# Kernel tuning notes

Hardware: AMD Instinct MI355X
Metric: run time of the kernel (lower is better)

## Reference

```python
import jax, jax.numpy as jnp
import numpy as np

NEG_SLOPE = 0.2  # PyG GATConv default leaky_relu negative_slope


def gat_conv(x, edge_index, W, att_src, att_dst, bias, heads, out_ch):
    """PyG GATConv (add_self_loops=False, concat=True, dropout disabled)."""
    N = x.shape[0]
    src, dst = edge_index[0], edge_index[1]
    h = (x @ W).reshape(N, heads, out_ch)               # [N,H,C]
    a_src = jnp.einsum('nhc,hc->nh', h, att_src)        # [N,H]
    a_dst = jnp.einsum('nhc,hc->nh', h, att_dst)        # [N,H]
    e = jax.nn.leaky_relu(a_src[src] + a_dst[dst], NEG_SLOPE)  # [E,H]
    # segment softmax over edges grouped by destination node
    e_max = jax.ops.segment_max(e, dst, num_segments=N)  # [N,H]
    e_exp = jnp.exp(e - e_max[dst])
    denom = jax.ops.segment_sum(e_exp, dst, num_segments=N)
    alpha = e_exp / (denom[dst] + 1e-16)                 # [E,H]
    msg = h[src] * alpha[:, :, None]                     # [E,H,C]
    out = jax.ops.segment_sum(msg, dst, num_segments=N)  # [N,H,C]
    return out.reshape(N, heads * out_ch) + bias


def setup_inputs() -> dict:
    key = jax.random.key(0)
    ks = jax.random.split(key, 10)
    N, E, F_IN, H, C1, OUT = 50000, 1600000, 256, 8, 8, 64
    s = 0.1
    return {
        'x': jax.random.normal(ks[0], (N, F_IN), jnp.float32),
        'edge_index': jax.random.randint(ks[1], (2, E), 0, N, jnp.int64),
        'W1': jax.random.normal(ks[2], (F_IN, H * C1), jnp.float32) * s,
        'att_src1': jax.random.normal(ks[3], (H, C1), jnp.float32) * s,
        'att_dst1': jax.random.normal(ks[4], (H, C1), jnp.float32) * s,
        'bias1': jax.random.normal(ks[5], (H * C1,), jnp.float32) * s,
        'W2': jax.random.normal(ks[6], (H * C1, OUT), jnp.float32) * s,
        'att_src2': jax.random.normal(ks[7], (1, OUT), jnp.float32) * s,
        'att_dst2': jax.random.normal(ks[8], (1, OUT), jnp.float32) * s,
        'bias2': jax.random.normal(ks[9], (OUT,), jnp.float32) * s,
    }


def reference(x, edge_index, W1, att_src1, att_dst1, bias1, W2, att_src2, att_dst2, bias2):
    # GAT.forward, eval mode with disable_dropout=True (no dropout, no loss)
    h = gat_conv(x, edge_index, W1, att_src1, att_dst1, bias1, heads=8, out_ch=8)
    h = jax.nn.elu(h)
    h = gat_conv(h, edge_index, W2, att_src2, att_dst2, bias2, heads=1, out_ch=64)
    return jax.nn.log_softmax(h, axis=1)
```

## Files before the change

kernel.cpp:

```cpp
#include <hip/hip_runtime.h>
#include <math.h>

#define LRELU 0.2f
#define BSH 7
#define BSZ (1 << BSH)
#define CH 8192
#define ECH 2048
#define GB 10
#define CAP 5120

typedef __attribute__((ext_vector_type(8))) short bf16x8;
typedef __attribute__((ext_vector_type(4))) float f32x4;

static __device__ __forceinline__ float bf2f(unsigned int u16) {
    union { unsigned int i; float f; } c; c.i = u16 << 16; return c.f;
}
static __device__ __forceinline__ unsigned short f2bf(float f) {
    union { float f; unsigned int i; } c; c.f = f;
    unsigned int x = c.i;
    return (unsigned short)((x + 0x7fffu + ((x >> 16) & 1u)) >> 16);
}


__global__ __launch_bounds__(256) void k_prep(const float* __restrict__ W1,
                                              const float* __restrict__ W2,
                                              const float* __restrict__ as2in,
                                              const float* __restrict__ ad2in,
                                              unsigned short* __restrict__ Wt1,
                                              unsigned short* __restrict__ Wt2,
                                              unsigned short* __restrict__ h1b,
                                              unsigned short* __restrict__ gb,
                                              float* __restrict__ w2s,
                                              float* __restrict__ w2d,
                                              int* __restrict__ bcur,
                                              int N, int NB) {
    int idx = blockIdx.x * 256 + threadIdx.x;
    if (idx < 16384) {
        int n = idx >> 8, k = idx & 255;
        Wt1[idx] = f2bf(W1[k * 64 + n]);
    } else if (idx < 16384 + 4096) {
        int j = idx - 16384;
        int n = j >> 6, k = j & 63;
        Wt2[j] = f2bf(W2[k * 64 + n]);
    } else if (idx >= 20480 && idx < 20544) {
        h1b[(size_t)N * 64 + (idx - 20480)] = 0;
    } else if (idx >= 20544 && idx < 20608) {
        gb[(size_t)N * 64 + (idx - 20544)] = 0;
    } else if (idx >= 20608 && idx < 20672) {
        int c = idx - 20608;
        float s = 0.f;
#pragma unroll
        for (int n = 0; n < 64; ++n) s += W2[c * 64 + n] * as2in[n];
        w2s[c] = s;
    } else if (idx >= 20672 && idx < 20736) {
        int c = idx - 20672;
        float s = 0.f;
#pragma unroll
        for (int n = 0; n < 64; ++n) s += W2[c * 64 + n] * ad2in[n];
        w2d[c] = s;
    } else if (idx >= 20736 && idx < 20736 + NB) {
        int b = idx - 20736;
        bcur[b] = b * CAP;
    }
}


__global__ __launch_bounds__(256) void k_mid(const int* __restrict__ src,
                                             const int* __restrict__ dstArr,
                                             int E, int NB,
                                             int* __restrict__ bcur,
                                             unsigned* __restrict__ pairs,
                                             const float* __restrict__ X,
                                             const unsigned short* __restrict__ Wt,
                                             const float* __restrict__ attd,
                                             int N, unsigned short* __restrict__ Hb,
                                             float* __restrict__ adst,
                                             int nchunk) {
    __shared__ short Xl[64 * 256];
    __shared__ int cnt2[512];
    int t = threadIdx.x;
    if ((int)blockIdx.x < nchunk) {
        int* lds_d = (int*)Xl;
        int e0 = blockIdx.x * CH;
        int e1 = e0 + CH; if (e1 > E) e1 = E;
        int n = e1 - e0;
        for (int b = t; b < 512; b += 256) cnt2[b] = 0;
        __syncthreads();
        for (int i = t; i < n; i += 256) {
            int d = dstArr[e0 + i];
            lds_d[i] = d;
            atomicAdd(&cnt2[d >> BSH], 1);
        }
        __syncthreads();
        for (int b = t; b < NB; b += 256) {
            int c = cnt2[b];
            cnt2[b] = c ? atomicAdd(&bcur[b], c) : 0;
        }
        __syncthreads();
        for (int i = t; i < n; i += 256) {
            int d = lds_d[i];
            int p = atomicAdd(&cnt2[d >> BSH], 1);
            pairs[p] = ((unsigned)src[e0 + i] << BSH) | (unsigned)(d & (BSZ - 1));
        }
        return;
    }
    int bx = (int)blockIdx.x - nchunk;
    int l = t & 63, w = t >> 6;
    int rblk = bx * 64;

    int half = l >> 5;
    int c8 = (l & 31) * 8;
#pragma unroll
    for (int i = 0; i < 8; ++i) {
        int rl = w * 16 + i * 2 + half;
        int row = rblk + rl;
        float4 x0 = {0.f, 0.f, 0.f, 0.f}, x1 = {0.f, 0.f, 0.f, 0.f};
        if (row < N) {
            x0 = *reinterpret_cast<const float4*>(X + (size_t)row * 256 + c8);
            x1 = *reinterpret_cast<const float4*>(X + (size_t)row * 256 + c8 + 4);
        }
        bf16x8 p;
        p[0] = (short)f2bf(x0.x); p[1] = (short)f2bf(x0.y);
        p[2] = (short)f2bf(x0.z); p[3] = (short)f2bf(x0.w);
        p[4] = (short)f2bf(x1.x); p[5] = (short)f2bf(x1.y);
        p[6] = (short)f2bf(x1.z); p[7] = (short)f2bf(x1.w);
        int g = (l & 31) ^ (rl & 7);
        *reinterpret_cast<bf16x8*>(&Xl[rl * 256 + g * 8]) = p;
    }
    __syncthreads();

    int m = l & 15, quad = l >> 4;
    int rl = w * 16 + m;
    f32x4 acc0 = {0.f, 0.f, 0.f, 0.f}, acc1 = acc0, acc2 = acc0, acc3 = acc0;
#pragma unroll
    for (int tt = 0; tt < 8; ++tt) {
        int g = (tt * 4 + quad) ^ (m & 7);
        bf16x8 a = *reinterpret_cast<const bf16x8*>(&Xl[rl * 256 + g * 8]);
        int kk = tt * 32 + quad * 8;
        bf16x8 b0 = *reinterpret_cast<const bf16x8*>(&Wt[(0 * 16 + m) * 256 + kk]);
        bf16x8 b1 = *reinterpret_cast<const bf16x8*>(&Wt[(1 * 16 + m) * 256 + kk]);
        bf16x8 b2 = *reinterpret_cast<const bf16x8*>(&Wt[(2 * 16 + m) * 256 + kk]);
        bf16x8 b3 = *reinterpret_cast<const bf16x8*>(&Wt[(3 * 16 + m) * 256 + kk]);
        acc0 = __builtin_amdgcn_mfma_f32_16x16x32_bf16(a, b0, acc0, 0, 0, 0);
        acc1 = __builtin_amdgcn_mfma_f32_16x16x32_bf16(a, b1, acc1, 0, 0, 0);
        acc2 = __builtin_amdgcn_mfma_f32_16x16x32_bf16(a, b2, acc2, 0, 0, 0);
        acc3 = __builtin_amdgcn_mfma_f32_16x16x32_bf16(a, b3, acc3, 0, 0, 0);
    }

    int r0 = rblk + w * 16;
    f32x4 accs[4] = {acc0, acc1, acc2, acc3};
#pragma unroll
    for (int nt = 0; nt < 4; ++nt) {
        int cn = nt * 16 + m;
        float av_d = attd[cn];
#pragma unroll
        for (int r = 0; r < 4; ++r) {
            int row = r0 + quad * 4 + r;
            float hv = accs[nt][r];
            if (row < N) Hb[(size_t)row * 64 + cn] = f2bf(hv);
            float vd = hv * av_d;
            vd += __shfl_xor(vd, 1, 64); vd += __shfl_xor(vd, 2, 64); vd += __shfl_xor(vd, 4, 64);
            if ((m & 7) == 0 && row < N) {
                adst[row * 8 + (cn >> 3)] = vd;
            }
        }
    }
}


__global__ __launch_bounds__(256) void k_bucket(const int* __restrict__ bcur,
                                                const unsigned* __restrict__ pairs,
                                                int N, int* __restrict__ rowptr,
                                                int* __restrict__ rowend,
                                                int* __restrict__ col) {
    __shared__ int pairsS[CAP];
    __shared__ int cnt[BSZ];
    __shared__ int cur[BSZ];
    int t = threadIdx.x;
    int b = blockIdx.x;
    int dlo = b << BSH;
    int dhi = dlo + BSZ; if (dhi > N) dhi = N;
    int nd = dhi - dlo;
    int jb = b * CAP;
    int je = bcur[b];
    int n = je - jb;
    if (t < BSZ) cnt[t] = 0;
    __syncthreads();
    for (int i = t; i < n; i += 256) {
        int pk = (int)pairs[jb + i];
        pairsS[i] = pk;
        atomicAdd(&cnt[pk & (BSZ - 1)], 1);
    }
    __syncthreads();
    if (t < 64) {
        int v0 = cnt[t], v1 = cnt[64 + t];
        int i0 = v0;
#pragma unroll
        for (int off = 1; off < 64; off <<= 1) {
            int q = __shfl_up(i0, off, 64);
            if (t >= off) i0 += q;
        }
        int tot0 = __shfl(i0, 63, 64);
        int i1 = v1;
#pragma unroll
        for (int off = 1; off < 64; off <<= 1) {
            int q = __shfl_up(i1, off, 64);
            if (t >= off) i1 += q;
        }
        int e0x = jb + i0 - v0;
        int e1x = jb + tot0 + i1 - v1;
        cur[t] = e0x;
        cur[64 + t] = e1x;
        if (t < nd) { rowptr[dlo + t] = e0x; rowend[dlo + t] = jb + i0; }
        if (64 + t < nd) { rowptr[dlo + 64 + t] = e1x; rowend[dlo + 64 + t] = jb + tot0 + i1; }
    }
    __syncthreads();
    for (int i = t; i < n; i += 256) {
        int pk = pairsS[i];
        int p = atomicAdd(&cur[pk & (BSZ - 1)], 1);
        col[p] = pk >> BSH;
    }
}


__global__ __launch_bounds__(256) void k_gather1f(const int* __restrict__ rowptr,
                                                  const int* __restrict__ rowend,
                                                  const int* __restrict__ col,
                                                  const uint4* __restrict__ Hb8,
                                                  const float* __restrict__ adst,
                                                  const float* __restrict__ attS,
                                                  const float* __restrict__ bias,
                                                  const unsigned short* __restrict__ Wt2,
                                                  const float* __restrict__ w2d,
                                                  int N,
                                                  unsigned short* __restrict__ Gb,
                                                  float* __restrict__ ad2) {
    __shared__ int colS[ECH];
    __shared__ short h2l[32 * 64];
    int t = threadIdx.x;
    int gid = t >> 3, sub = t & 7;
    int d0 = blockIdx.x * 32;
    int dend = d0 + 32; if (dend > N) dend = N;
    int d = d0 + gid;
    int dok = (d < dend);
    int dc = dok ? d : d0;
    int jb = rowptr[dc];
    int je = rowend[dc];
    if (!dok) { jb = 0; je = 0; }
    float adv = dok ? adst[dc * 8 + sub] : 0.f;
    float aS[8];
#pragma unroll
    for (int c = 0; c < 8; ++c) aS[c] = attS[sub * 8 + c];
    int ebeg = rowptr[d0];
    int eend = rowend[dend - 1];

    float acc[8] = {0.f, 0.f, 0.f, 0.f, 0.f, 0.f, 0.f, 0.f};
    float denom = 0.f;
    for (int cb = ebeg; cb < eend; cb += ECH) {
        int ce = cb + ECH; if (ce > eend) ce = eend;
        int n = ce - cb;
        __syncthreads();
        for (int i = t; i < n; i += 256) colS[i] = col[cb + i];
        __syncthreads();
        int lo = (jb > cb) ? jb : cb;
        int hi = (je < ce) ? je : ce;
        for (int u = lo; u < hi; u += GB) {
            uint4 hv8[GB];
#pragma unroll
            for (int q = 0; q < GB; ++q) {
                int uu = u + q;
                int s = (uu < hi) ? colS[uu - cb] : N;
                hv8[q] = Hb8[(size_t)s * 8 + sub];
            }
            __builtin_amdgcn_sched_barrier(0);
#pragma unroll
            for (int q = 0; q < GB; ++q) {
                uint4 hv = hv8[q];
                float f0 = bf2f(hv.x & 0xffffu), f1 = bf2f(hv.x >> 16);
                float f2 = bf2f(hv.y & 0xffffu), f3 = bf2f(hv.y >> 16);
                float f4 = bf2f(hv.z & 0xffffu), f5 = bf2f(hv.z >> 16);
                float f6 = bf2f(hv.w & 0xffffu), f7 = bf2f(hv.w >> 16);
                float ps = f0 * aS[0];
                ps = fmaf(f1, aS[1], ps); ps = fmaf(f2, aS[2], ps);
                ps = fmaf(f3, aS[3], ps); ps = fmaf(f4, aS[4], ps);
                ps = fmaf(f5, aS[5], ps); ps = fmaf(f6, aS[6], ps);
                ps = fmaf(f7, aS[7], ps);
                float e = ps + adv;
                e = (e > 0.f) ? e : LRELU * e;
                float wgt = ((u + q) < hi) ? __expf(e) : 0.f;
                denom += wgt;
                acc[0] = fmaf(wgt, f0, acc[0]); acc[1] = fmaf(wgt, f1, acc[1]);
                acc[2] = fmaf(wgt, f2, acc[2]); acc[3] = fmaf(wgt, f3, acc[3]);
                acc[4] = fmaf(wgt, f4, acc[4]); acc[5] = fmaf(wgt, f5, acc[5]);
                acc[6] = fmaf(wgt, f6, acc[6]); acc[7] = fmaf(wgt, f7, acc[7]);
            }
        }
    }

    float invd = 1.f / (denom + 1e-16f);
    float v[8];
#pragma unroll
    for (int c = 0; c < 8; ++c) {
        float x = fmaf(acc[c], invd, bias[sub * 8 + c]);
        v[c] = (x > 0.f) ? x : expm1f(x);
    }
    float vd = 0.f;
#pragma unroll
    for (int c = 0; c < 8; ++c) vd = fmaf(v[c], w2d[sub * 8 + c], vd);
    vd += __shfl_xor(vd, 1, 64); vd += __shfl_xor(vd, 2, 64); vd += __shfl_xor(vd, 4, 64);
    if (dok && sub == 0) ad2[d] = vd;

    bf16x8 p;
#pragma unroll
    for (int c = 0; c < 8; ++c) p[c] = (short)f2bf(v[c]);
    *reinterpret_cast<bf16x8*>(&h2l[gid * 64 + (sub ^ (gid & 7)) * 8]) = p;
    __syncthreads();

    int l = t & 63, w = t >> 6;
    int m = l & 15, quad = l >> 4;
    int mt = w & 1;
    int ntb = (w >> 1) * 2;
    int r = mt * 16 + m;
    f32x4 g0 = {0.f, 0.f, 0.f, 0.f}, g1 = g0;
#pragma unroll
    for (int tt = 0; tt < 2; ++tt) {
        bf16x8 a = *reinterpret_cast<const bf16x8*>(
            &h2l[r * 64 + ((tt * 4 + quad) ^ (r & 7)) * 8]);
        int kk = tt * 32 + quad * 8;
        bf16x8 b0 = *reinterpret_cast<const bf16x8*>(&Wt2[((ntb + 0) * 16 + m) * 64 + kk]);
        bf16x8 b1 = *reinterpret_cast<const bf16x8*>(&Wt2[((ntb + 1) * 16 + m) * 64 + kk]);
        g0 = __builtin_amdgcn_mfma_f32_16x16x32_bf16(a, b0, g0, 0, 0, 0);
        g1 = __builtin_amdgcn_mfma_f32_16x16x32_bf16(a, b1, g1, 0, 0, 0);
    }
    f32x4 gs[2] = {g0, g1};
#pragma unroll
    for (int nt = 0; nt < 2; ++nt) {
        int cn = (ntb + nt) * 16 + m;
#pragma unroll
        for (int rr = 0; rr < 4; ++rr) {
            int dr = d0 + mt * 16 + quad * 4 + rr;
            if (dr < N) Gb[(size_t)dr * 64 + cn] = f2bf(gs[nt][rr]);
        }
    }
}


__global__ __launch_bounds__(256) void k_gather2(const int* __restrict__ rowptr,
                                                 const int* __restrict__ rowend,
                                                 const int* __restrict__ col,
                                                 const uint4* __restrict__ Gb8,
                                                 const float* __restrict__ adst,
                                                 const float* __restrict__ w2s,
                                                 const float* __restrict__ bias,
                                                 int N,
                                                 float* __restrict__ out) {
    __shared__ int colS[ECH];
    int t = threadIdx.x;
    int gid = t >> 3, sub = t & 7;
    int d0 = blockIdx.x * 32;
    int dend = d0 + 32; if (dend > N) dend = N;
    int d = d0 + gid;
    int dok = (d < dend);
    int dc = dok ? d : d0;
    int jb = rowptr[dc];
    int je = rowend[dc];
    if (!dok) { jb = 0; je = 0; }
    float adv = dok ? adst[dc] : 0.f;
    float wS[8];
#pragma unroll
    for (int c = 0; c < 8; ++c) wS[c] = w2s[sub * 8 + c];
    int ebeg = rowptr[d0];
    int eend = rowend[dend - 1];

    float acc[8] = {0.f, 0.f, 0.f, 0.f, 0.f, 0.f, 0.f, 0.f};
    float denom = 0.f;
    for (int cb = ebeg; cb < eend; cb += ECH) {
        int ce = cb + ECH; if (ce > eend) ce = eend;
        int n = ce - cb;
        __syncthreads();
        for (int i = t; i < n; i += 256) colS[i] = col[cb + i];
        __syncthreads();
        int lo = (jb > cb) ? jb : cb;
        int hi = (je < ce) ? je : ce;
        for (int u = lo; u < hi; u += GB) {
            uint4 hv8[GB];
#pragma unroll
            for (int q = 0; q < GB; ++q) {
                int uu = u + q;
                int s = (uu < hi) ? colS[uu - cb] : N;
                hv8[q] = Gb8[(size_t)s * 8 + sub];
            }
            __builtin_amdgcn_sched_barrier(0);
#pragma unroll
            for (int q = 0; q < GB; ++q) {
                uint4 hv = hv8[q];
                float f0 = bf2f(hv.x & 0xffffu), f1 = bf2f(hv.x >> 16);
                float f2 = bf2f(hv.y & 0xffffu), f3 = bf2f(hv.y >> 16);
                float f4 = bf2f(hv.z & 0xffffu), f5 = bf2f(hv.z >> 16);
                float f6 = bf2f(hv.w & 0xffffu), f7 = bf2f(hv.w >> 16);
                float ps = f0 * wS[0];
                ps = fmaf(f1, wS[1], ps); ps = fmaf(f2, wS[2], ps);
                ps = fmaf(f3, wS[3], ps); ps = fmaf(f4, wS[4], ps);
                ps = fmaf(f5, wS[5], ps); ps = fmaf(f6, wS[6], ps);
                ps = fmaf(f7, wS[7], ps);
                ps += __shfl_xor(ps, 1, 64);
                ps += __shfl_xor(ps, 2, 64);
                ps += __shfl_xor(ps, 4, 64);
                float e = ps + adv;
                e = (e > 0.f) ? e : LRELU * e;
                float wgt = ((u + q) < hi) ? __expf(e) : 0.f;
                denom += wgt;
                acc[0] = fmaf(wgt, f0, acc[0]); acc[1] = fmaf(wgt, f1, acc[1]);
                acc[2] = fmaf(wgt, f2, acc[2]); acc[3] = fmaf(wgt, f3, acc[3]);
                acc[4] = fmaf(wgt, f4, acc[4]); acc[5] = fmaf(wgt, f5, acc[5]);
                acc[6] = fmaf(wgt, f6, acc[6]); acc[7] = fmaf(wgt, f7, acc[7]);
            }
        }
    }
    float invd = 1.f / (denom + 1e-16f);
    float v[8];
#pragma unroll
    for (int c = 0; c < 8; ++c) v[c] = fmaf(acc[c], invd, bias[sub * 8 + c]);
    float m = v[0];
#pragma unroll
    for (int c = 1; c < 8; ++c) m = fmaxf(m, v[c]);
    m = fmaxf(m, __shfl_xor(m, 1, 64));
    m = fmaxf(m, __shfl_xor(m, 2, 64));
    m = fmaxf(m, __shfl_xor(m, 4, 64));
    float se = 0.f;
#pragma unroll
    for (int c = 0; c < 8; ++c) se += __expf(v[c] - m);
    se += __shfl_xor(se, 1, 64);
    se += __shfl_xor(se, 2, 64);
    se += __shfl_xor(se, 4, 64);
    float ls = m + __logf(se);
    if (dok) {
        float4 o0, o1;
        o0.x = v[0] - ls; o0.y = v[1] - ls; o0.z = v[2] - ls; o0.w = v[3] - ls;
        o1.x = v[4] - ls; o1.y = v[5] - ls; o1.z = v[6] - ls; o1.w = v[7] - ls;
        *reinterpret_cast<float4*>(&out[(size_t)d * 64 + sub * 8]) = o0;
        *reinterpret_cast<float4*>(&out[(size_t)d * 64 + sub * 8 + 4]) = o1;
    }
}


extern "C" void kernel_launch(void* const* d_in, const int* in_sizes, int n_in,
                              void* d_out, int out_size, void* d_ws, size_t ws_size,
                              hipStream_t stream) {
    const float* x   = (const float*)d_in[0];
    const int*   ei  = (const int*)d_in[1];
    const float* W1  = (const float*)d_in[2];
    const float* as1 = (const float*)d_in[3];
    const float* ad1 = (const float*)d_in[4];
    const float* b1  = (const float*)d_in[5];
    const float* W2  = (const float*)d_in[6];
    const float* as2 = (const float*)d_in[7];
    const float* ad2 = (const float*)d_in[8];
    const float* b2  = (const float*)d_in[9];
    float* out = (float*)d_out;

    const int N = in_sizes[0] / 256;
    const int E = in_sizes[1] / 2;
    const int* src = ei;
    const int* dst = ei + E;
    const int NB = (N + BSZ - 1) >> BSH;
    const int nchunk = (E + CH - 1) / CH;

    char* ws = (char*)d_ws;
    size_t off = 0;
    auto alloc = [&](size_t bytes) -> void* {
        void* p = ws + off;
        off = (off + bytes + 255) & ~(size_t)255;
        return p;
    };
    int*      bcur   = (int*)alloc((size_t)NB * 4);
    int*      rowptr = (int*)alloc((size_t)N * 4);
    int*      rowend = (int*)alloc((size_t)N * 4);
    int*      col    = (int*)alloc((size_t)NB * CAP * 4);
    unsigned* pairs  = (unsigned*)alloc((size_t)NB * CAP * 4);
    unsigned short* wt1 = (unsigned short*)alloc(64 * 256 * 2);
    unsigned short* wt2 = (unsigned short*)alloc(64 * 64 * 2);
    unsigned short* h1b = (unsigned short*)alloc((size_t)(N + 1) * 64 * 2);
    float* a_d1   = (float*)alloc((size_t)N * 8 * 4);
    unsigned short* gb  = (unsigned short*)alloc((size_t)(N + 1) * 64 * 2);
    float* a_d2   = (float*)alloc((size_t)N * 4);
    float* w2s    = (float*)alloc(64 * 4);
    float* w2d    = (float*)alloc(64 * 4);
    (void)ws_size; (void)n_in; (void)out_size;

    int prep_blocks = (20736 + NB + 255) / 256;
    k_prep<<<prep_blocks, 256, 0, stream>>>(W1, W2, as2, ad2, wt1, wt2,
                                            h1b, gb, w2s, w2d, bcur, N, NB);

    int gblk = (N + 63) / 64;
    k_mid<<<nchunk + gblk, 256, 0, stream>>>(src, dst, E, NB, bcur, pairs,
                                             x, wt1, ad1, N, h1b, a_d1, nchunk);

    k_bucket<<<NB, 256, 0, stream>>>(bcur, pairs, N, rowptr, rowend, col);

    int gather_blocks = (N + 31) / 32;
    k_gather1f<<<gather_blocks, 256, 0, stream>>>(rowptr, rowend, col,
                                                  (const uint4*)h1b,
                                                  a_d1, as1, b1, wt2, w2d,
                                                  N, gb, a_d2);

    k_gather2<<<gather_blocks, 256, 0, stream>>>(rowptr, rowend, col,
                                                 (const uint4*)gb,
                                                 a_d2, w2s, b2, N, out);
}
```

Measured before the change: 225.9 us.

## Fuse per-bucket CSR sort into both gather kernels and drop k_bucket

Removes the separate bucketing kernel that built rowptr, rowend and col arrays in global memory. Each gather block now owns a 32-node destination bucket: it loads that bucket's packed (src, dst) pairs, counts and prefix-sums them in LDS, and scatters the source indices into an LDS column list before gathering. This saves a kernel launch and the global write and re-read of the CSR arrays. In exchange the in-LDS sort is done twice (once per layer), k_mid issues more global bucket-counter atomics because there are more, smaller buckets, and the fixed per-bucket capacity of 1408 assumes no bucket overflows.

```diff
diff --git a/kernel.cpp b/kernel.cpp
--- a/kernel.cpp
+++ b/kernel.cpp
@@ -2,12 +2,12 @@
 #include <math.h>
 
 #define LRELU 0.2f
-#define BSH 7
+#define BSH 5
 #define BSZ (1 << BSH)
 #define CH 8192
-#define ECH 2048
 #define GB 10
-#define CAP 5120
+#define CAP 1408
+#define NBMAX 1600
 
 typedef __attribute__((ext_vector_type(8))) short bf16x8;
 typedef __attribute__((ext_vector_type(4))) float f32x4;
@@ -77,14 +77,14 @@
                                              float* __restrict__ adst,
                                              int nchunk) {
     __shared__ short Xl[64 * 256];
-    __shared__ int cnt2[512];
+    __shared__ int cnt2[NBMAX];
     int t = threadIdx.x;
     if ((int)blockIdx.x < nchunk) {
         int* lds_d = (int*)Xl;
         int e0 = blockIdx.x * CH;
         int e1 = e0 + CH; if (e1 > E) e1 = E;
         int n = e1 - e0;
-        for (int b = t; b < 512; b += 256) cnt2[b] = 0;
+        for (int b = t; b < NBMAX; b += 256) cnt2[b] = 0;
         __syncthreads();
         for (int i = t; i < n; i += 256) {
             int d = dstArr[e0 + i];
@@ -168,64 +168,8 @@
 }
 
 
-__global__ __launch_bounds__(256) void k_bucket(const int* __restrict__ bcur,
-                                                const unsigned* __restrict__ pairs,
-                                                int N, int* __restrict__ rowptr,
-                                                int* __restrict__ rowend,
-                                                int* __restrict__ col) {
-    __shared__ int pairsS[CAP];
-    __shared__ int cnt[BSZ];
-    __shared__ int cur[BSZ];
-    int t = threadIdx.x;
-    int b = blockIdx.x;
-    int dlo = b << BSH;
-    int dhi = dlo + BSZ; if (dhi > N) dhi = N;
-    int nd = dhi - dlo;
-    int jb = b * CAP;
-    int je = bcur[b];
-    int n = je - jb;
-    if (t < BSZ) cnt[t] = 0;
-    __syncthreads();
-    for (int i = t; i < n; i += 256) {
-        int pk = (int)pairs[jb + i];
-        pairsS[i] = pk;
-        atomicAdd(&cnt[pk & (BSZ - 1)], 1);
-    }
-    __syncthreads();
-    if (t < 64) {
-        int v0 = cnt[t], v1 = cnt[64 + t];
-        int i0 = v0;
-#pragma unroll
-        for (int off = 1; off < 64; off <<= 1) {
-            int q = __shfl_up(i0, off, 64);
-            if (t >= off) i0 += q;
-        }
-        int tot0 = __shfl(i0, 63, 64);
-        int i1 = v1;
-#pragma unroll
-        for (int off = 1; off < 64; off <<= 1) {
-            int q = __shfl_up(i1, off, 64);
-            if (t >= off) i1 += q;
-        }
-        int e0x = jb + i0 - v0;
-        int e1x = jb + tot0 + i1 - v1;
-        cur[t] = e0x;
-        cur[64 + t] = e1x;
-        if (t < nd) { rowptr[dlo + t] = e0x; rowend[dlo + t] = jb + i0; }
-        if (64 + t < nd) { rowptr[dlo + 64 + t] = e1x; rowend[dlo + 64 + t] = jb + tot0 + i1; }
-    }
-    __syncthreads();
-    for (int i = t; i < n; i += 256) {
-        int pk = pairsS[i];
-        int p = atomicAdd(&cur[pk & (BSZ - 1)], 1);
-        col[p] = pk >> BSH;
-    }
-}
-
-
-__global__ __launch_bounds__(256) void k_gather1f(const int* __restrict__ rowptr,
-                                                  const int* __restrict__ rowend,
-                                                  const int* __restrict__ col,
+__global__ __launch_bounds__(256) void k_gather1f(const int* __restrict__ bcur,
+                                                  const unsigned* __restrict__ pairs,
                                                   const uint4* __restrict__ Hb8,
                                                   const float* __restrict__ adst,
                                                   const float* __restrict__ attS,
@@ -235,65 +179,86 @@
                                                   int N,
                                                   unsigned short* __restrict__ Gb,
                                                   float* __restrict__ ad2) {
-    __shared__ int colS[ECH];
+    __shared__ int pairsS[CAP];
+    __shared__ int colT[CAP];
+    __shared__ int cntS[BSZ];
+    __shared__ int baseS[BSZ];
+    __shared__ int curS[BSZ];
     __shared__ short h2l[32 * 64];
     int t = threadIdx.x;
     int gid = t >> 3, sub = t & 7;
-    int d0 = blockIdx.x * 32;
-    int dend = d0 + 32; if (dend > N) dend = N;
+    int b = blockIdx.x;
+    int d0 = b << BSH;
     int d = d0 + gid;
-    int dok = (d < dend);
+    int dok = (d < N);
     int dc = dok ? d : d0;
-    int jb = rowptr[dc];
-    int je = rowend[dc];
-    if (!dok) { jb = 0; je = 0; }
     float adv = dok ? adst[dc * 8 + sub] : 0.f;
     float aS[8];
 #pragma unroll
     for (int c = 0; c < 8; ++c) aS[c] = attS[sub * 8 + c];
-    int ebeg = rowptr[d0];
-    int eend = rowend[dend - 1];
+
+    int jb = b * CAP;
+    int n = bcur[b] - jb;
+    if (t < BSZ) cntS[t] = 0;
+    __syncthreads();
+    for (int i = t; i < n; i += 256) {
+        int pk = (int)pairs[jb + i];
+        pairsS[i] = pk;
+        atomicAdd(&cntS[pk & (BSZ - 1)], 1);
+    }
+    __syncthreads();
+    if (t < 64) {
+        int v = (t < BSZ) ? cntS[t] : 0;
+        int inc = v;
+#pragma unroll
+        for (int off = 1; off < BSZ; off <<= 1) {
+            int q = __shfl_up(inc, off, 64);
+            if (t >= off) inc += q;
+        }
+        if (t < BSZ) { baseS[t] = inc - v; curS[t] = inc - v; }
+    }
+    __syncthreads();
+    for (int i = t; i < n; i += 256) {
+        int pk = pairsS[i];
+        int p = atomicAdd(&curS[pk & (BSZ - 1)], 1);
+        colT[p] = pk >> BSH;
+    }
+    __syncthreads();
+
+    int lo = baseS[gid];
+    int hi = lo + cntS[gid];
 
     float acc[8] = {0.f, 0.f, 0.f, 0.f, 0.f, 0.f, 0.f, 0.f};
     float denom = 0.f;
-    for (int cb = ebeg; cb < eend; cb += ECH) {
-        int ce = cb + ECH; if (ce > eend) ce = eend;
-        int n = ce - cb;
-        __syncthreads();
-        for (int i = t; i < n; i += 256) colS[i] = col[cb + i];
-        __syncthreads();
-        int lo = (jb > cb) ? jb : cb;
-        int hi = (je < ce) ? je : ce;
-        for (int u = lo; u < hi; u += GB) {
-            uint4 hv8[GB];
-#pragma unroll
-            for (int q = 0; q < GB; ++q) {
-                int uu = u + q;
-                int s = (uu < hi) ? colS[uu - cb] : N;
-                hv8[q] = Hb8[(size_t)s * 8 + sub];
-            }
-            __builtin_amdgcn_sched_barrier(0);
-#pragma unroll
-            for (int q = 0; q < GB; ++q) {
-                uint4 hv = hv8[q];
-                float f0 = bf2f(hv.x & 0xffffu), f1 = bf2f(hv.x >> 16);
-                float f2 = bf2f(hv.y & 0xffffu), f3 = bf2f(hv.y >> 16);
-                float f4 = bf2f(hv.z & 0xffffu), f5 = bf2f(hv.z >> 16);
-                float f6 = bf2f(hv.w & 0xffffu), f7 = bf2f(hv.w >> 16);
-                float ps = f0 * aS[0];
-                ps = fmaf(f1, aS[1], ps); ps = fmaf(f2, aS[2], ps);
-                ps = fmaf(f3, aS[3], ps); ps = fmaf(f4, aS[4], ps);
-                ps = fmaf(f5, aS[5], ps); ps = fmaf(f6, aS[6], ps);
-                ps = fmaf(f7, aS[7], ps);
-                float e = ps + adv;
-                e = (e > 0.f) ? e : LRELU * e;
-                float wgt = ((u + q) < hi) ? __expf(e) : 0.f;
-                denom += wgt;
-                acc[0] = fmaf(wgt, f0, acc[0]); acc[1] = fmaf(wgt, f1, acc[1]);
-                acc[2] = fmaf(wgt, f2, acc[2]); acc[3] = fmaf(wgt, f3, acc[3]);
-                acc[4] = fmaf(wgt, f4, acc[4]); acc[5] = fmaf(wgt, f5, acc[5]);
-                acc[6] = fmaf(wgt, f6, acc[6]); acc[7] = fmaf(wgt, f7, acc[7]);
-            }
+    for (int u = lo; u < hi; u += GB) {
+        uint4 hv8[GB];
+#pragma unroll
+        for (int q = 0; q < GB; ++q) {
+            int uu = u + q;
+            int s = (uu < hi) ? colT[uu] : N;
+            hv8[q] = Hb8[(size_t)s * 8 + sub];
+        }
+        __builtin_amdgcn_sched_barrier(0);
+#pragma unroll
+        for (int q = 0; q < GB; ++q) {
+            uint4 hv = hv8[q];
+            float f0 = bf2f(hv.x & 0xffffu), f1 = bf2f(hv.x >> 16);
+            float f2 = bf2f(hv.y & 0xffffu), f3 = bf2f(hv.y >> 16);
+            float f4 = bf2f(hv.z & 0xffffu), f5 = bf2f(hv.z >> 16);
+            float f6 = bf2f(hv.w & 0xffffu), f7 = bf2f(hv.w >> 16);
+            float ps = f0 * aS[0];
+            ps = fmaf(f1, aS[1], ps); ps = fmaf(f2, aS[2], ps);
+            ps = fmaf(f3, aS[3], ps); ps = fmaf(f4, aS[4], ps);
+            ps = fmaf(f5, aS[5], ps); ps = fmaf(f6, aS[6], ps);
+            ps = fmaf(f7, aS[7], ps);
+            float e = ps + adv;
+            e = (e > 0.f) ? e : LRELU * e;
+            float wgt = ((u + q) < hi) ? __expf(e) : 0.f;
+            denom += wgt;
+            acc[0] = fmaf(wgt, f0, acc[0]); acc[1] = fmaf(wgt, f1, acc[1]);
+            acc[2] = fmaf(wgt, f2, acc[2]); acc[3] = fmaf(wgt, f3, acc[3]);
+            acc[4] = fmaf(wgt, f4, acc[4]); acc[5] = fmaf(wgt, f5, acc[5]);
+            acc[6] = fmaf(wgt, f6, acc[6]); acc[7] = fmaf(wgt, f7, acc[7]);
         }
     }
 
@@ -345,76 +310,96 @@
 }
 
 
-__global__ __launch_bounds__(256) void k_gather2(const int* __restrict__ rowptr,
-                                                 const int* __restrict__ rowend,
-                                                 const int* __restrict__ col,
+__global__ __launch_bounds__(256) void k_gather2(const int* __restrict__ bcur,
+                                                 const unsigned* __restrict__ pairs,
                                                  const uint4* __restrict__ Gb8,
                                                  const float* __restrict__ adst,
                                                  const float* __restrict__ w2s,
                                                  const float* __restrict__ bias,
                                                  int N,
                                                  float* __restrict__ out) {
-    __shared__ int colS[ECH];
+    __shared__ int pairsS[CAP];
+    __shared__ int colT[CAP];
+    __shared__ int cntS[BSZ];
+    __shared__ int baseS[BSZ];
+    __shared__ int curS[BSZ];
     int t = threadIdx.x;
     int gid = t >> 3, sub = t & 7;
-    int d0 = blockIdx.x * 32;
-    int dend = d0 + 32; if (dend > N) dend = N;
+    int b = blockIdx.x;
+    int d0 = b << BSH;
     int d = d0 + gid;
-    int dok = (d < dend);
+    int dok = (d < N);
     int dc = dok ? d : d0;
-    int jb = rowptr[dc];
-    int je = rowend[dc];
-    if (!dok) { jb = 0; je = 0; }
     float adv = dok ? adst[dc] : 0.f;
     float wS[8];
 #pragma unroll
     for (int c = 0; c < 8; ++c) wS[c] = w2s[sub * 8 + c];
-    int ebeg = rowptr[d0];
-    int eend = rowend[dend - 1];
+
+    int jb = b * CAP;
+    int n = bcur[b] - jb;
+    if (t < BSZ) cntS[t] = 0;
+    __syncthreads();
+    for (int i = t; i < n; i += 256) {
+        int pk = (int)pairs[jb + i];
+        pairsS[i] = pk;
+        atomicAdd(&cntS[pk & (BSZ - 1)], 1);
+    }
+    __syncthreads();
+    if (t < 64) {
+        int v = (t < BSZ) ? cntS[t] : 0;
+        int inc = v;
+#pragma unroll
+        for (int off = 1; off < BSZ; off <<= 1) {
+            int q = __shfl_up(inc, off, 64);
+            if (t >= off) inc += q;
+        }
+        if (t < BSZ) { baseS[t] = inc - v; curS[t] = inc - v; }
+    }
+    __syncthreads();
+    for (int i = t; i < n; i += 256) {
+        int pk = pairsS[i];
+        int p = atomicAdd(&curS[pk & (BSZ - 1)], 1);
+        colT[p] = pk >> BSH;
+    }
+    __syncthreads();
+
+    int lo = baseS[gid];
+    int hi = lo + cntS[gid];
 
     float acc[8] = {0.f, 0.f, 0.f, 0.f, 0.f, 0.f, 0.f, 0.f};
     float denom = 0.f;
-    for (int cb = ebeg; cb < eend; cb += ECH) {
-        int ce = cb + ECH; if (ce > eend) ce = eend;
-        int n = ce - cb;
-        __syncthreads();
-        for (int i = t; i < n; i += 256) colS[i] = col[cb + i];
-        __syncthreads();
-        int lo = (jb > cb) ? jb : cb;
-        int hi = (je < ce) ? je : ce;
-        for (int u = lo; u < hi; u += GB) {
-            uint4 hv8[GB];
-#pragma unroll
-            for (int q = 0; q < GB; ++q) {
-                int uu = u + q;
-                int s = (uu < hi) ? colS[uu - cb] : N;
-                hv8[q] = Gb8[(size_t)s * 8 + sub];
-            }
-            __builtin_amdgcn_sched_barrier(0);
-#pragma unroll
-            for (int q = 0; q < GB; ++q) {
-                uint4 hv = hv8[q];
-                float f0 = bf2f(hv.x & 0xffffu), f1 = bf2f(hv.x >> 16);
-                float f2 = bf2f(hv.y & 0xffffu), f3 = bf2f(hv.y >> 16);
-                float f4 = bf2f(hv.z & 0xffffu), f5 = bf2f(hv.z >> 16);
-                float f6 = bf2f(hv.w & 0xffffu), f7 = bf2f(hv.w >> 16);
-                float ps = f0 * wS[0];
-                ps = fmaf(f1, wS[1], ps); ps = fmaf(f2, wS[2], ps);
-                ps = fmaf(f3, wS[3], ps); ps = fmaf(f4, wS[4], ps);
-                ps = fmaf(f5, wS[5], ps); ps = fmaf(f6, wS[6], ps);
-                ps = fmaf(f7, wS[7], ps);
-                ps += __shfl_xor(ps, 1, 64);
-                ps += __shfl_xor(ps, 2, 64);
-                ps += __shfl_xor(ps, 4, 64);
-                float e = ps + adv;
-                e = (e > 0.f) ? e : LRELU * e;
-                float wgt = ((u + q) < hi) ? __expf(e) : 0.f;
-                denom += wgt;
-                acc[0] = fmaf(wgt, f0, acc[0]); acc[1] = fmaf(wgt, f1, acc[1]);
-                acc[2] = fmaf(wgt, f2, acc[2]); acc[3] = fmaf(wgt, f3, acc[3]);
-                acc[4] = fmaf(wgt, f4, acc[4]); acc[5] = fmaf(wgt, f5, acc[5]);
-                acc[6] = fmaf(wgt, f6, acc[6]); acc[7] = fmaf(wgt, f7, acc[7]);
-            }
+    for (int u = lo; u < hi; u += GB) {
+        uint4 hv8[GB];
+#pragma unroll
+        for (int q = 0; q < GB; ++q) {
+            int uu = u + q;
+            int s = (uu < hi) ? colT[uu] : N;
+            hv8[q] = Gb8[(size_t)s * 8 + sub];
+        }
+        __builtin_amdgcn_sched_barrier(0);
+#pragma unroll
+        for (int q = 0; q < GB; ++q) {
+            uint4 hv = hv8[q];
+            float f0 = bf2f(hv.x & 0xffffu), f1 = bf2f(hv.x >> 16);
+            float f2 = bf2f(hv.y & 0xffffu), f3 = bf2f(hv.y >> 16);
+            float f4 = bf2f(hv.z & 0xffffu), f5 = bf2f(hv.z >> 16);
+            float f6 = bf2f(hv.w & 0xffffu), f7 = bf2f(hv.w >> 16);
+            float ps = f0 * wS[0];
+            ps = fmaf(f1, wS[1], ps); ps = fmaf(f2, wS[2], ps);
+            ps = fmaf(f3, wS[3], ps); ps = fmaf(f4, wS[4], ps);
+            ps = fmaf(f5, wS[5], ps); ps = fmaf(f6, wS[6], ps);
+            ps = fmaf(f7, wS[7], ps);
+            ps += __shfl_xor(ps, 1, 64);
+            ps += __shfl_xor(ps, 2, 64);
+            ps += __shfl_xor(ps, 4, 64);
+            float e = ps + adv;
+            e = (e > 0.f) ? e : LRELU * e;
+            float wgt = ((u + q) < hi) ? __expf(e) : 0.f;
+            denom += wgt;
+            acc[0] = fmaf(wgt, f0, acc[0]); acc[1] = fmaf(wgt, f1, acc[1]);
+            acc[2] = fmaf(wgt, f2, acc[2]); acc[3] = fmaf(wgt, f3, acc[3]);
+            acc[4] = fmaf(wgt, f4, acc[4]); acc[5] = fmaf(wgt, f5, acc[5]);
+            acc[6] = fmaf(wgt, f6, acc[6]); acc[7] = fmaf(wgt, f7, acc[7]);
         }
     }
     float invd = 1.f / (denom + 1e-16f);
@@ -474,9 +459,6 @@
         return p;
     };
     int*      bcur   = (int*)alloc((size_t)NB * 4);
-    int*      rowptr = (int*)alloc((size_t)N * 4);
-    int*      rowend = (int*)alloc((size_t)N * 4);
-    int*      col    = (int*)alloc((size_t)NB * CAP * 4);
     unsigned* pairs  = (unsigned*)alloc((size_t)NB * CAP * 4);
     unsigned short* wt1 = (unsigned short*)alloc(64 * 256 * 2);
     unsigned short* wt2 = (unsigned short*)alloc(64 * 64 * 2);
@@ -496,15 +478,10 @@
     k_mid<<<nchunk + gblk, 256, 0, stream>>>(src, dst, E, NB, bcur, pairs,
                                              x, wt1, ad1, N, h1b, a_d1, nchunk);
 
-    k_bucket<<<NB, 256, 0, stream>>>(bcur, pairs, N, rowptr, rowend, col);
-
-    int gather_blocks = (N + 31) / 32;
-    k_gather1f<<<gather_blocks, 256, 0, stream>>>(rowptr, rowend, col,
-                                                  (const uint4*)h1b,
-                                                  a_d1, as1, b1, wt2, w2d,
-                                                  N, gb, a_d2);
-
-    k_gather2<<<gather_blocks, 256, 0, stream>>>(rowptr, rowend, col,
-                                                 (const uint4*)gb,
-                                                 a_d2, w2s, b2, N, out);
-}
+    k_gather1f<<<NB, 256, 0, stream>>>(bcur, pairs, (const uint4*)h1b,
+                                       a_d1, as1, b1, wt2, w2d,
+                                       N, gb, a_d2);
+
+    k_gather2<<<NB, 256, 0, stream>>>(bcur, pairs, (const uint4*)gb,
+                                      a_d2, w2s, b2, N, out);
+}
```

Measured after the change: 224.6 us, median of 2. No clear change (-0.6%).
